# Performance work log

Hardware: AMD Instinct MI355X
Metric: run time of the kernel (lower is better)

Reference implementation:

```python
import jax, jax.numpy as jnp
import numpy as np

NUM_HEADS = 8


def _conv3x3(x, w, b):
    # x: (B, C, H, W); w: (O, I, 3, 3) -> (B, O, H, W), stride 1, SAME padding
    y = jax.lax.conv_general_dilated(
        x, w, window_strides=(1, 1), padding='SAME',
        dimension_numbers=('NCHW', 'OIHW', 'NCHW'))
    return y + b[None, :, None, None]


def setup_inputs() -> dict:
    key = jax.random.key(0)
    ks = jax.random.split(key, 7)
    bs, mc, C, H, W = 2, 5, 640, 32, 32
    s = 0.02  # init scale for weights
    return {
        'x': jax.random.normal(ks[0], (bs, mc, C, H, W), jnp.float32),
        'wq': jax.random.normal(ks[1], (C, C, 3, 3), jnp.float32) * s,
        'bq': jnp.zeros((C,), jnp.float32),
        'wk': jax.random.normal(ks[2], (C, C, 3, 3), jnp.float32) * s,
        'bk': jnp.zeros((C,), jnp.float32),
        'wv': jax.random.normal(ks[3], (C, C, 3, 3), jnp.float32) * s,
        'bv': jnp.zeros((C,), jnp.float32),
        'w_proj': jax.random.normal(ks[4], (C, C), jnp.float32) * s,
        'b_proj': jnp.zeros((C,), jnp.float32),
    }


def reference(x, wq, bq, wk, bk, wv, bv, w_proj, b_proj):
    bs, mc, C, H, W = x.shape
    N = H * W
    nh = NUM_HEADS
    hd = C // nh
    scale = hd ** -0.5

    xf = x.reshape(bs * mc, C, H, W)

    def proj(w, b):
        # conv -> (bs, mc, nh, hd, N) -> (bs, mc, nh, N, hd)
        y = _conv3x3(xf, w, b).reshape(bs, mc, nh, hd, N)
        return y.transpose(0, 1, 2, 4, 3)

    q = proj(wq, bq)
    k = proj(wk, bk)
    v = proj(wv, bv)

    attn = jax.nn.softmax(jnp.einsum('bmhnd,bmhkd->bmhnk', q, k) * scale, axis=-1)
    o = jnp.einsum('bmhnk,bmhkd->bmhnd', attn, v)  # (bs, mc, nh, N, hd)

    # permute(0,3,1,2,4).reshape(bs, N, mc*C) then split back to (bs, N, mc, C)
    o = o.transpose(0, 3, 1, 2, 4).reshape(bs, N, mc, C)
    o = jnp.einsum('bnmc,dc->bnmd', o, w_proj) + b_proj  # Linear(C, C)
    return o.reshape(bs, N, mc * C)
```

## Files before the change

kernel.cpp:

```cpp
#include <hip/hip_runtime.h>

typedef _Float16 half_t;
typedef _Float16 half8 __attribute__((ext_vector_type(8)));
typedef _Float16 half4 __attribute__((ext_vector_type(4)));
typedef float floatx4 __attribute__((ext_vector_type(4)));
typedef unsigned int u32;

#define MFMA32(a,b,c) __builtin_amdgcn_mfma_f32_16x16x32_f16(a,b,c,0,0,0)
#define MFMA16(a,b,c) __builtin_amdgcn_mfma_f32_16x16x16f16(a,b,c,0,0,0)

#define XPAD_ELEMS (10u*34*34*640)
#define WR_ELEMS   (3u*9*640*640)
#define WP_ELEMS   (640u*640)
#define QKV_ELEMS  (10u*8*1024*80)
#define O_ELEMS    (10u*1024*640)

__device__ __forceinline__ void load16_lds(half_t* lds, const half_t* g) {
  __builtin_amdgcn_global_load_lds((const __attribute__((address_space(1))) u32*)g,
                                   (__attribute__((address_space(3))) u32*)lds,
                                   16, 0, 0);
}

__global__ __launch_bounds__(256) void k_convert_x(const float* __restrict__ x,
                                                   half_t* __restrict__ xpad) {
  const int img = blockIdx.x >> 5, y = blockIdx.x & 31;
  const float* src = x + (size_t)img*640*1024 + y*32;
  half_t* dst = xpad + (size_t)img*34*34*640;
  for (int i = threadIdx.x; i < 640*32; i += 256) {
    int xx = i / 640, c = i - xx*640;
    float v = src[(size_t)c*1024 + xx];
    dst[((size_t)(y+1)*34 + xx + 1)*640 + c] = (half_t)v;
  }
}

__global__ __launch_bounds__(256) void k_convert_w(const float* __restrict__ wq,
                                                   const float* __restrict__ wk,
                                                   const float* __restrict__ wv,
                                                   const float* __restrict__ wp,
                                                   half_t* __restrict__ wr2,
                                                   half_t* __restrict__ wp16) {
  const int p = blockIdx.y, row = blockIdx.x;
  if (p < 3) {
    const float* W = (p == 0) ? wq : (p == 1) ? wk : wv;
    for (int i = threadIdx.x; i < 5760; i += 256) {
      int t = i / 640, ci = i - t*640;
      wr2[(((size_t)p*640 + row)*9 + t)*640 + ci] = (half_t)W[((size_t)row*640 + ci)*9 + t];
    }
  } else {
    for (int i = threadIdx.x; i < 640; i += 256)
      wp16[(size_t)row*640 + i] = (half_t)wp[(size_t)row*640 + i];
  }
}

__global__ __launch_bounds__(256) void k_conv(const half_t* __restrict__ xpad,
                                              const half_t* __restrict__ wr2,
                                              const float* __restrict__ bq,
                                              const float* __restrict__ bk,
                                              const float* __restrict__ bv,
                                              half_t* __restrict__ qo,
                                              half_t* __restrict__ ko,
                                              half_t* __restrict__ vo) {
  __shared__ __align__(16) half_t sX[2][816*8];
  __shared__ __align__(16) half_t sW[4][512*8];
  const int tid = threadIdx.x;
  const int lane = tid & 63, wv = tid >> 6;
  const int l15 = lane & 15, lq = lane >> 4, lq16 = lq*16;
  const int mt = blockIdx.x, nt = blockIdx.y;
  const int proj = blockIdx.z / 10, img = blockIdx.z - proj*10;

  const half_t* xg = xpad + ((size_t)img*34*34 + (size_t)mt*4*34)*640;
  const half_t* wg = wr2 + ((size_t)proj*640 + nt*128)*5760;

  int xsrc[4], wsrc[2];
#pragma unroll
  for (int kk = 0; kk < 4; ++kk) {
    int idx = kk*256 + tid;
    int row = idx >> 2, slot = idx & 3;
    int chunk = slot ^ ((row >> 1) & 3);
    xsrc[kk] = row*640 + chunk*8;
  }
#pragma unroll
  for (int kk = 0; kk < 2; ++kk) {
    int idx = kk*256 + tid;
    int row = idx >> 2, slot = idx & 3;
    int chunk = slot ^ ((row >> 1) & 3);
    wsrc[kk] = row*5760 + chunk*8;
  }

  const int wrow = (wv >> 1)*64, wcol = (wv & 1)*64;
  int arow0[4];
#pragma unroll
  for (int fr = 0; fr < 4; ++fr) {
    int p = wrow + fr*16 + l15;
    arow0[fr] = (p >> 5)*34 + (p & 31);
  }
  int bboff[4];
#pragma unroll
  for (int fc = 0; fc < 4; ++fc) {
    int r = wcol + fc*16 + l15;
    bboff[fc] = (r << 6) + (lq16 ^ (((r >> 1) & 3) << 4));
  }

#pragma unroll
  for (int kk = 0; kk < 4; ++kk)
    if (kk < 3 || tid < 48)
      load16_lds(sX[0] + (size_t)(kk*256 + wv*64)*8, xg + xsrc[kk]);
#pragma unroll
  for (int st = 0; st < 3; ++st) {
    load16_lds(sW[st] + (size_t)(wv*64)*8,       wg + wsrc[0] + st*640);
    load16_lds(sW[st] + (size_t)(256 + wv*64)*8, wg + wsrc[1] + st*640);
  }
  asm volatile("s_waitcnt vmcnt(0)" ::: "memory");
  __builtin_amdgcn_s_barrier();

  floatx4 acc[4][4] = {};
  half8 Av[4], Aw[4], Bv[4], Bw[4];

  {
    const char* sXc = (const char*)sX[0];
    const char* sWc = (const char*)sW[0];
#pragma unroll
    for (int fr = 0; fr < 4; ++fr) {
      int r = arow0[fr];
      Av[fr] = *(const half8*)(sXc + (r << 6) + (lq16 ^ (((r >> 1) & 3) << 4)));
    }
#pragma unroll
    for (int fc = 0; fc < 4; ++fc) Aw[fc] = *(const half8*)(sWc + bboff[fc]);
  }

#define STEP(T, g, CURv, CURw, NXTv, NXTw) do {                                    \
    const int s_ = 9*(g) + (T);                                                    \
    if (s_ + 3 <= 179) {                                                           \
      const int t3 = ((T) + 3) % 9;                                                \
      const int g3 = (g) + ((T) + 3) / 9;                                          \
      const int k0 = t3*640 + g3*32;                                               \
      half_t* wd = sW[(s_ + 3) & 3];                                               \
      load16_lds(wd + (size_t)(wv*64)*8,       wg + wsrc[0] + k0);                 \
      load16_lds(wd + (size_t)(256 + wv*64)*8, wg + wsrc[1] + k0);                 \
    }                                                                              \
    if ((T) == 5 && (g) < 19) {                                                    \
      half_t* xd = sX[((g) + 1) & 1];                                              \
      _Pragma("unroll")                                                            \
      for (int kk = 0; kk < 4; ++kk)                                               \
        if (kk < 3 || tid < 48)                                                    \
          load16_lds(xd + (size_t)(kk*256 + wv*64)*8, xg + xsrc[kk] + ((g)+1)*32); \
    }                                                                              \
    if ((T) >= 5 && (T) <= 7 && (g) < 19) {                                        \
      if (wv == 0) asm volatile("s_waitcnt vmcnt(8)" ::: "memory");                \
      else         asm volatile("s_waitcnt vmcnt(7)" ::: "memory");                \
    } else if (s_ <= 176) asm volatile("s_waitcnt vmcnt(4)" ::: "memory");         \
    else if (s_ == 177)   asm volatile("s_waitcnt vmcnt(2)" ::: "memory");         \
    else                  asm volatile("s_waitcnt vmcnt(0)" ::: "memory");         \
    __builtin_amdgcn_s_barrier();                                                  \
    __builtin_amdgcn_sched_barrier(0);                                             \
    if (s_ < 179) {                                                                \
      const int tn = ((T) + 1) % 9;                                                \
      const int gn = (g) + ((T) + 1) / 9;                                          \
      const int TRn = (tn/3)*34 + (tn - (tn/3)*3);                                 \
      const char* sXc = (const char*)sX[gn & 1];                                   \
      const char* sWc = (const char*)sW[(s_ + 1) & 3];                             \
      _Pragma("unroll")                                                            \
      for (int fr = 0; fr < 4; ++fr) {                                             \
        int r = arow0[fr] + TRn;                                                   \
        NXTv[fr] = *(const half8*)(sXc + (r << 6) + (lq16 ^ (((r >> 1) & 3) << 4)));\
      }                                                                            \
      _Pragma("unroll")                                                            \
      for (int fc = 0; fc < 4; ++fc) NXTw[fc] = *(const half8*)(sWc + bboff[fc]);  \
    }                                                                              \
    __builtin_amdgcn_sched_barrier(0);                                             \
    __builtin_amdgcn_s_setprio(1);                                                 \
    _Pragma("unroll")                                                              \
    for (int fr = 0; fr < 4; ++fr)                                                 \
      _Pragma("unroll")                                                            \
      for (int fc = 0; fc < 4; ++fc)                                               \
        acc[fr][fc] = MFMA32(CURv[fr], CURw[fc], acc[fr][fc]);                     \
    __builtin_amdgcn_s_setprio(0);                                                 \
  } while (0)

  for (int gg = 0; gg < 20; gg += 2) {
    STEP(0, gg, Av, Aw, Bv, Bw);
    STEP(1, gg, Bv, Bw, Av, Aw);
    STEP(2, gg, Av, Aw, Bv, Bw);
    STEP(3, gg, Bv, Bw, Av, Aw);
    STEP(4, gg, Av, Aw, Bv, Bw);
    STEP(5, gg, Bv, Bw, Av, Aw);
    STEP(6, gg, Av, Aw, Bv, Bw);
    STEP(7, gg, Bv, Bw, Av, Aw);
    STEP(8, gg, Av, Aw, Bv, Bw);
    STEP(0, gg+1, Bv, Bw, Av, Aw);
    STEP(1, gg+1, Av, Aw, Bv, Bw);
    STEP(2, gg+1, Bv, Bw, Av, Aw);
    STEP(3, gg+1, Av, Aw, Bv, Bw);
    STEP(4, gg+1, Bv, Bw, Av, Aw);
    STEP(5, gg+1, Av, Aw, Bv, Bw);
    STEP(6, gg+1, Bv, Bw, Av, Aw);
    STEP(7, gg+1, Av, Aw, Bv, Bw);
    STEP(8, gg+1, Bv, Bw, Av, Aw);
  }
#undef STEP

  const float* bias = (proj == 0) ? bq : (proj == 1) ? bk : bv;
#pragma unroll
  for (int fc = 0; fc < 4; ++fc) {
    int co = nt*128 + wcol + fc*16 + l15;
    float bb = bias[co];
    int hh = co / 80;
    int d = co - hh*80;
#pragma unroll
    for (int fr = 0; fr < 4; ++fr)
#pragma unroll
      for (int j = 0; j < 4; ++j) {
        int n = mt*128 + wrow + fr*16 + lq*4 + j;
        float val = acc[fr][fc][j] + bb;
        if (proj == 0)      qo[((size_t)(img*8 + hh)*1024 + n)*80 + d] = (half_t)(val * 0.11180339887498949f);
        else if (proj == 1) ko[((size_t)(img*8 + hh)*1024 + n)*80 + d] = (half_t)val;
        else                vo[((size_t)(img*8 + hh)*80 + d)*1024 + n] = (half_t)val;
      }
  }
}

__global__ __launch_bounds__(256) void k_attn(const half_t* __restrict__ qg_,
                                              const half_t* __restrict__ kg_,
                                              const half_t* __restrict__ vg_,
                                              half_t* __restrict__ og_) {
  __shared__ __align__(16) half_t sQ[128*80];
  __shared__ __align__(16) half_t sK[64*80];
  __shared__ __align__(16) half_t sV[80*64];
  __shared__ __align__(16) half_t sP[128*64];
  const int tid = threadIdx.x, lane = tid & 63, wv = tid >> 6;
  const int l15 = lane & 15, lq = lane >> 4;
  const int qt = blockIdx.x, gh = blockIdx.y;
  const half_t* qg = qg_ + ((size_t)gh*1024 + qt*128)*80;
  const half_t* kg = kg_ + (size_t)gh*1024*80;
  const half_t* vg = vg_ + (size_t)gh*80*1024;

#pragma unroll
  for (int kk = 0; kk < 5; ++kk)
    load16_lds(sQ + (size_t)(kk*256 + wv*64)*8, qg + (size_t)(kk*256 + tid)*8);

  float mrow[2][4], lrow[2][4];
  floatx4 oacc[2][5] = {};
#pragma unroll
  for (int fr = 0; fr < 2; ++fr)
#pragma unroll
    for (int j = 0; j < 4; ++j) { mrow[fr][j] = -1e30f; lrow[fr][j] = 0.f; }

  for (int kt = 0; kt < 16; ++kt) {
    __syncthreads();
#pragma unroll
    for (int kk = 0; kk < 3; ++kk) {
      int c = kk*256 + tid;
      if (c < 640) {
        int row = c / 10, cw = c - row*10;
        load16_lds(sK + (size_t)(kk*256 + wv*64)*8,
                   kg + ((size_t)kt*64 + row)*80 + cw*8);
      }
    }
#pragma unroll
    for (int kk = 0; kk < 3; ++kk) {
      int c = kk*256 + tid;
      if (c < 640) {
        load16_lds(sV + (size_t)(kk*256 + wv*64)*8,
                   vg + (size_t)(c >> 3)*1024 + kt*64 + (c & 7)*8);
      }
    }
    __syncthreads();

    const char* sQb = (const char*)sQ;
    const char* sKb = (const char*)sK;
    half8 qa0[2], qa1[2]; half4 qa2[2];
#pragma unroll
    for (int fr = 0; fr < 2; ++fr) {
      int r = wv*32 + fr*16 + l15;
      qa0[fr] = *(const half8*)(sQb + r*160 + lq*16);
      qa1[fr] = *(const half8*)(sQb + r*160 + 64 + lq*16);
      qa2[fr] = *(const half4*)(sQb + r*160 + 128 + lq*8);
    }
    floatx4 s[2][4];
#pragma unroll
    for (int fc = 0; fc < 4; ++fc) {
      int key = fc*16 + l15;
      half8 kb0 = *(const half8*)(sKb + key*160 + lq*16);
      half8 kb1 = *(const half8*)(sKb + key*160 + 64 + lq*16);
      half4 kb2 = *(const half4*)(sKb + key*160 + 128 + lq*8);
#pragma unroll
      for (int fr = 0; fr < 2; ++fr) {
        floatx4 t = {0.f, 0.f, 0.f, 0.f};
        t = MFMA16(qa2[fr], kb2, t);
        t = MFMA32(qa0[fr], kb0, t);
        t = MFMA32(qa1[fr], kb1, t);
        s[fr][fc] = t;
      }
    }

    float corr[2][4], psum[2][4];
#pragma unroll
    for (int fr = 0; fr < 2; ++fr)
#pragma unroll
      for (int j = 0; j < 4; ++j) {
        float mx = fmaxf(fmaxf(s[fr][0][j], s[fr][1][j]), fmaxf(s[fr][2][j], s[fr][3][j]));
        mx = fmaxf(mx, __shfl_xor(mx, 1));
        mx = fmaxf(mx, __shfl_xor(mx, 2));
        mx = fmaxf(mx, __shfl_xor(mx, 4));
        mx = fmaxf(mx, __shfl_xor(mx, 8));
        float mn = fmaxf(mrow[fr][j], mx);
        corr[fr][j] = __expf(mrow[fr][j] - mn);
        mrow[fr][j] = mn;
        psum[fr][j] = 0.f;
      }
#pragma unroll
    for (int fc = 0; fc < 4; ++fc)
#pragma unroll
      for (int fr = 0; fr < 2; ++fr)
#pragma unroll
        for (int j = 0; j < 4; ++j) {
          float p = __expf(s[fr][fc][j] - mrow[fr][j]);
          psum[fr][j] += p;
          sP[(size_t)(wv*32 + fr*16 + lq*4 + j)*64 + fc*16 + l15] = (half_t)p;
        }
#pragma unroll
    for (int fr = 0; fr < 2; ++fr)
#pragma unroll
      for (int j = 0; j < 4; ++j) {
        float t2 = psum[fr][j];
        t2 += __shfl_xor(t2, 1);
        t2 += __shfl_xor(t2, 2);
        t2 += __shfl_xor(t2, 4);
        t2 += __shfl_xor(t2, 8);
        lrow[fr][j] = lrow[fr][j]*corr[fr][j] + t2;
      }
#pragma unroll
    for (int fr = 0; fr < 2; ++fr)
#pragma unroll
      for (int fc = 0; fc < 5; ++fc)
#pragma unroll
        for (int j = 0; j < 4; ++j)
          oacc[fr][fc][j] *= corr[fr][j];

    __syncthreads();

    const char* sPb = (const char*)sP;
    const char* sVb = (const char*)sV;
    half8 pa[2][2];
#pragma unroll
    for (int fr = 0; fr < 2; ++fr) {
      int r = wv*32 + fr*16 + l15;
#pragma unroll
      for (int ks = 0; ks < 2; ++ks)
        pa[fr][ks] = *(const half8*)(sPb + r*128 + ks*64 + lq*16);
    }
#pragma unroll
    for (int fc = 0; fc < 5; ++fc)
#pragma unroll
      for (int ks = 0; ks < 2; ++ks) {
        half8 vb = *(const half8*)(sVb + (fc*16 + l15)*128 + ks*64 + lq*16);
#pragma unroll
        for (int fr = 0; fr < 2; ++fr)
          oacc[fr][fc] = MFMA32(pa[fr][ks], vb, oacc[fr][fc]);
      }
  }

  const int img = gh >> 3, hh = gh & 7;
  half_t* og = og_ + ((size_t)img*1024 + qt*128)*640 + hh*80;
#pragma unroll
  for (int fr = 0; fr < 2; ++fr)
#pragma unroll
    for (int j = 0; j < 4; ++j) {
      int n = wv*32 + fr*16 + lq*4 + j;
      float inv = 1.f / lrow[fr][j];
#pragma unroll
      for (int fc = 0; fc < 5; ++fc)
        og[(size_t)n*640 + fc*16 + l15] = (half_t)(oacc[fr][fc][j] * inv);
    }
}

__global__ __launch_bounds__(256) void k_proj(const half_t* __restrict__ oa,
                                              const half_t* __restrict__ wp,
                                              const float* __restrict__ bp,
                                              float* __restrict__ out) {
  __shared__ __align__(16) half_t sA[128*32];
  __shared__ __align__(16) half_t sB[128*32];
  const int tid = threadIdx.x, lane = tid & 63, wv = tid >> 6;
  const int l15 = lane & 15, lq = lane >> 4;
  const int mt = blockIdx.x, nt = blockIdx.y, img = blockIdx.z;
  const int bb = img / 5, mm = img - bb*5;
  const half_t* ag = oa + ((size_t)img*1024 + mt*128)*640;
  const half_t* bg = wp + (size_t)nt*128*640;
  const int wrow = (wv >> 1)*64, wcol = (wv & 1)*64;
  floatx4 acc[4][4] = {};
  for (int g = 0; g < 20; ++g) {
    __syncthreads();
#pragma unroll
    for (int kk = 0; kk < 2; ++kk) {
      int c = kk*256 + tid;
      load16_lds(sA + (size_t)(kk*256 + wv*64)*8, ag + (size_t)(c >> 2)*640 + g*32 + (c & 3)*8);
      load16_lds(sB + (size_t)(kk*256 + wv*64)*8, bg + (size_t)(c >> 2)*640 + g*32 + (c & 3)*8);
    }
    __syncthreads();
    const char* sAb = (const char*)sA;
    const char* sBb = (const char*)sB;
    half8 av[4], bw[4];
#pragma unroll
    for (int fr = 0; fr < 4; ++fr) av[fr] = *(const half8*)(sAb + (wrow + fr*16 + l15)*64 + lq*16);
#pragma unroll
    for (int fc = 0; fc < 4; ++fc) bw[fc] = *(const half8*)(sBb + (wcol + fc*16 + l15)*64 + lq*16);
#pragma unroll
    for (int fr = 0; fr < 4; ++fr)
#pragma unroll
      for (int fc = 0; fc < 4; ++fc)
        acc[fr][fc] = MFMA32(av[fr], bw[fc], acc[fr][fc]);
  }
  float* og = out + ((size_t)bb*1024 + mt*128)*3200 + mm*640 + nt*128;
#pragma unroll
  for (int fc = 0; fc < 4; ++fc) {
    float bias = bp[nt*128 + wcol + fc*16 + l15];
#pragma unroll
    for (int fr = 0; fr < 4; ++fr)
#pragma unroll
      for (int j = 0; j < 4; ++j)
        og[(size_t)(wrow + fr*16 + lq*4 + j)*3200 + wcol + fc*16 + l15] = acc[fr][fc][j] + bias;
  }
}

extern "C" void kernel_launch(void* const* d_in, const int* in_sizes, int n_in,
                              void* d_out, int out_size, void* d_ws, size_t ws_size,
                              hipStream_t stream) {
  const float* x  = (const float*)d_in[0];
  const float* wq = (const float*)d_in[1];
  const float* bq = (const float*)d_in[2];
  const float* wk = (const float*)d_in[3];
  const float* bk = (const float*)d_in[4];
  const float* wv = (const float*)d_in[5];
  const float* bv = (const float*)d_in[6];
  const float* wp = (const float*)d_in[7];
  const float* bp = (const float*)d_in[8];
  float* out = (float*)d_out;

  half_t* xpad = (half_t*)d_ws;
  half_t* wr2  = xpad + XPAD_ELEMS;
  half_t* wp16 = wr2 + WR_ELEMS;
  half_t* q    = wp16 + WP_ELEMS;
  half_t* k    = q + QKV_ELEMS;
  half_t* v    = k + QKV_ELEMS;
  half_t* oa   = v + QKV_ELEMS;

  (void)hipMemsetAsync(xpad, 0, (size_t)XPAD_ELEMS*sizeof(half_t), stream);
  k_convert_x<<<320, 256, 0, stream>>>(x, xpad);
  k_convert_w<<<dim3(640, 4), 256, 0, stream>>>(wq, wk, wv, wp, wr2, wp16);
  k_conv<<<dim3(8, 5, 30), 256, 0, stream>>>(xpad, wr2, bq, bk, bv, q, k, v);
  k_attn<<<dim3(8, 80), 256, 0, stream>>>(q, k, v, oa);
  k_proj<<<dim3(8, 5, 10), 256, 0, stream>>>(oa, wp16, bp, out);
}
```

Baseline: 454.5 us.

## Shrink conv weight ring to 3 stages, add occupancy hint, XCD-aware block remap

The conv kernel's weight prefetch ring drops from 4 to 3 LDS buffers with a prefetch distance of 2, and the waitcnt schedule is retuned to match. A launch-bounds minimum of 4 blocks per CU is added. Both kernels switch to 1D grids with a remap that sends consecutive logical tiles to the same XCD. Together these aim for higher occupancy and better L2 locality, at the cost of a shorter prefetch lead and possible register pressure.

```diff
diff --git a/kernel.cpp b/kernel.cpp
--- a/kernel.cpp
+++ b/kernel.cpp
@@ -52,24 +52,29 @@
   }
 }
 
-__global__ __launch_bounds__(256) void k_conv(const half_t* __restrict__ xpad,
-                                              const half_t* __restrict__ wr2,
-                                              const float* __restrict__ bq,
-                                              const float* __restrict__ bk,
-                                              const float* __restrict__ bv,
-                                              half_t* __restrict__ qo,
-                                              half_t* __restrict__ ko,
-                                              half_t* __restrict__ vo) {
+__global__ __launch_bounds__(256, 4) void k_conv(const half_t* __restrict__ xpad,
+                                                 const half_t* __restrict__ wr2,
+                                                 const float* __restrict__ bq,
+                                                 const float* __restrict__ bk,
+                                                 const float* __restrict__ bv,
+                                                 half_t* __restrict__ qo,
+                                                 half_t* __restrict__ ko,
+                                                 half_t* __restrict__ vo) {
   __shared__ __align__(16) half_t sX[2][816*8];
-  __shared__ __align__(16) half_t sW[4][512*8];
+  __shared__ __align__(16) half_t sW[3][512*8];
   const int tid = threadIdx.x;
   const int lane = tid & 63, wv = tid >> 6;
   const int l15 = lane & 15, lq = lane >> 4, lq16 = lq*16;
-  const int mt = blockIdx.x, nt = blockIdx.y;
-  const int proj = blockIdx.z / 10, img = blockIdx.z - proj*10;
+  const int id = blockIdx.x;
+  const int wg = (id >> 3) + (id & 7)*150;
+  const int mt = wg & 7;
+  const int rest = wg >> 3;
+  const int nt = rest % 5;
+  const int z  = rest / 5;
+  const int proj = z / 10, img = z - proj*10;
 
   const half_t* xg = xpad + ((size_t)img*34*34 + (size_t)mt*4*34)*640;
-  const half_t* wg = wr2 + ((size_t)proj*640 + nt*128)*5760;
+  const half_t* wg_ = wr2 + ((size_t)proj*640 + nt*128)*5760;
 
   int xsrc[4], wsrc[2];
 #pragma unroll
@@ -106,11 +111,11 @@
     if (kk < 3 || tid < 48)
       load16_lds(sX[0] + (size_t)(kk*256 + wv*64)*8, xg + xsrc[kk]);
 #pragma unroll
-  for (int st = 0; st < 3; ++st) {
-    load16_lds(sW[st] + (size_t)(wv*64)*8,       wg + wsrc[0] + st*640);
-    load16_lds(sW[st] + (size_t)(256 + wv*64)*8, wg + wsrc[1] + st*640);
-  }
-  asm volatile("s_waitcnt vmcnt(0)" ::: "memory");
+  for (int st = 0; st < 2; ++st) {
+    load16_lds(sW[st] + (size_t)(wv*64)*8,       wg_ + wsrc[0] + st*640);
+    load16_lds(sW[st] + (size_t)(256 + wv*64)*8, wg_ + wsrc[1] + st*640);
+  }
+  asm volatile("s_waitcnt vmcnt(2)" ::: "memory");
   __builtin_amdgcn_s_barrier();
 
   floatx4 acc[4][4] = {};
@@ -130,13 +135,13 @@
 
 #define STEP(T, g, CURv, CURw, NXTv, NXTw) do {                                    \
     const int s_ = 9*(g) + (T);                                                    \
-    if (s_ + 3 <= 179) {                                                           \
-      const int t3 = ((T) + 3) % 9;                                                \
-      const int g3 = (g) + ((T) + 3) / 9;                                          \
-      const int k0 = t3*640 + g3*32;                                               \
-      half_t* wd = sW[(s_ + 3) & 3];                                               \
-      load16_lds(wd + (size_t)(wv*64)*8,       wg + wsrc[0] + k0);                 \
-      load16_lds(wd + (size_t)(256 + wv*64)*8, wg + wsrc[1] + k0);                 \
+    if (s_ + 2 <= 179) {                                                           \
+      const int t2 = ((T) + 2) % 9;                                                \
+      const int g2 = (g) + ((T) + 2) / 9;                                          \
+      const int k0 = t2*640 + g2*32;                                               \
+      half_t* wd = sW[((T) + 2) % 3];                                              \
+      load16_lds(wd + (size_t)(wv*64)*8,       wg_ + wsrc[0] + k0);                \
+      load16_lds(wd + (size_t)(256 + wv*64)*8, wg_ + wsrc[1] + k0);                \
     }                                                                              \
     if ((T) == 5 && (g) < 19) {                                                    \
       half_t* xd = sX[((g) + 1) & 1];                                              \
@@ -145,12 +150,14 @@
         if (kk < 3 || tid < 48)                                                    \
           load16_lds(xd + (size_t)(kk*256 + wv*64)*8, xg + xsrc[kk] + ((g)+1)*32); \
     }                                                                              \
-    if ((T) >= 5 && (T) <= 7 && (g) < 19) {                                        \
-      if (wv == 0) asm volatile("s_waitcnt vmcnt(8)" ::: "memory");                \
-      else         asm volatile("s_waitcnt vmcnt(7)" ::: "memory");                \
-    } else if (s_ <= 176) asm volatile("s_waitcnt vmcnt(4)" ::: "memory");         \
-    else if (s_ == 177)   asm volatile("s_waitcnt vmcnt(2)" ::: "memory");         \
-    else                  asm volatile("s_waitcnt vmcnt(0)" ::: "memory");         \
+    if (((T) == 5 || (T) == 6) && (g) < 19) {                                      \
+      if (wv == 0) asm volatile("s_waitcnt vmcnt(6)" ::: "memory");                \
+      else         asm volatile("s_waitcnt vmcnt(5)" ::: "memory");                \
+    } else if (((T) == 7 || (T) == 8) && (g) == 19) {                              \
+      asm volatile("s_waitcnt vmcnt(0)" ::: "memory");                             \
+    } else {                                                                       \
+      asm volatile("s_waitcnt vmcnt(2)" ::: "memory");                             \
+    }                                                                              \
     __builtin_amdgcn_s_barrier();                                                  \
     __builtin_amdgcn_sched_barrier(0);                                             \
     if (s_ < 179) {                                                                \
@@ -158,7 +165,7 @@
       const int gn = (g) + ((T) + 1) / 9;                                          \
       const int TRn = (tn/3)*34 + (tn - (tn/3)*3);                                 \
       const char* sXc = (const char*)sX[gn & 1];                                   \
-      const char* sWc = (const char*)sW[(s_ + 1) & 3];                             \
+      const char* sWc = (const char*)sW[((T) + 1) % 3];                            \
       _Pragma("unroll")                                                            \
       for (int fr = 0; fr < 4; ++fr) {                                             \
         int r = arow0[fr] + TRn;                                                   \
@@ -229,7 +236,9 @@
   __shared__ __align__(16) half_t sP[128*64];
   const int tid = threadIdx.x, lane = tid & 63, wv = tid >> 6;
   const int l15 = lane & 15, lq = lane >> 4;
-  const int qt = blockIdx.x, gh = blockIdx.y;
+  const int id = blockIdx.x;
+  const int wgb = (id >> 3) + (id & 7)*80;
+  const int qt = wgb & 7, gh = wgb >> 3;
   const half_t* qg = qg_ + ((size_t)gh*1024 + qt*128)*80;
   const half_t* kg = kg_ + (size_t)gh*1024*80;
   const half_t* vg = vg_ + (size_t)gh*80*1024;
@@ -447,7 +456,7 @@
   (void)hipMemsetAsync(xpad, 0, (size_t)XPAD_ELEMS*sizeof(half_t), stream);
   k_convert_x<<<320, 256, 0, stream>>>(x, xpad);
   k_convert_w<<<dim3(640, 4), 256, 0, stream>>>(wq, wk, wv, wp, wr2, wp16);
-  k_conv<<<dim3(8, 5, 30), 256, 0, stream>>>(xpad, wr2, bq, bk, bv, q, k, v);
-  k_attn<<<dim3(8, 80), 256, 0, stream>>>(q, k, v, oa);
+  k_conv<<<1200, 256, 0, stream>>>(xpad, wr2, bq, bk, bv, q, k, v);
+  k_attn<<<640, 256, 0, stream>>>(q, k, v, oa);
   k_proj<<<dim3(8, 5, 10), 256, 0, stream>>>(oa, wp16, bp, out);
 }
```

Measured after the change: 445.5 us. 2.0% less time.
